# Performance work log

Measured on AMD Instinct MI355X. Metric: run time of the kernel, lower is better.

The kernel has to match this reference:

```python
import jax, jax.numpy as jnp
import numpy as np

B, C, H, W = 16, 512, 32, 32
KC = C // 8  # key_channels = 64


def setup_inputs() -> dict:
    key = jax.random.key(0)
    ks = jax.random.split(key, 6)
    s_in = 1.0 / np.sqrt(C)
    return {
        "x": jax.random.normal(ks[0], (B, C, H, W), dtype=jnp.float32),
        "Wq": jax.random.normal(ks[1], (KC, C), dtype=jnp.float32) * s_in,
        "bq": jnp.zeros((KC,), dtype=jnp.float32),
        "Wk": jax.random.normal(ks[2], (KC, C), dtype=jnp.float32) * s_in,
        "bk": jnp.zeros((KC,), dtype=jnp.float32),
        "Wv": jax.random.normal(ks[3], (C, C), dtype=jnp.float32) * s_in,
        "bv": jnp.zeros((C,), dtype=jnp.float32),
        "Wo": jax.random.normal(ks[4], (C, C), dtype=jnp.float32) * s_in,
        "bo": jnp.zeros((C,), dtype=jnp.float32),
        "gamma": jnp.zeros((1,), dtype=jnp.float32),
    }


def reference(x, Wq, bq, Wk, bk, Wv, bv, Wo, bo, gamma):
    b, c, h, w = x.shape
    n = h * w
    kc = Wq.shape[0]
    xf = x.reshape(b, c, n)  # [B, C, N]
    # 1x1 convs == channel matmuls
    q = jnp.einsum('kc,bcn->bnk', Wq, xf) + bq  # [B, N, KC]
    k = jnp.einsum('kc,bcn->bkn', Wk, xf) + bk[None, :, None]  # [B, KC, N]
    v = jnp.einsum('vc,bcn->bnv', Wv, xf) + bv  # [B, N, C]
    scale = jnp.asarray(kc, x.dtype) ** -0.5
    att = jax.nn.softmax(jnp.einsum('bnk,bkm->bnm', q, k) * scale, axis=-1)  # [B, N, N]
    out = jnp.einsum('bnm,bmv->bnv', att, v)  # [B, N, C]
    out = jnp.einsum('cv,bnv->bcn', Wo, out) + bo[None, :, None]  # [B, C, N]
    out = gamma[0] * out + xf
    return out.reshape(b, c, h, w)
```

## Files before the change

kernel.cpp:

```cpp
#include <hip/hip_runtime.h>
#include <cstddef>


typedef unsigned short ushort_t;
typedef __attribute__((ext_vector_type(8))) short bf16x8;
typedef __attribute__((ext_vector_type(4))) float f32x4;
typedef __attribute__((ext_vector_type(2))) float f32x2;
typedef __attribute__((ext_vector_type(2))) unsigned u32x2;

#define QSCALE 0.18033688011112042f

__device__ __forceinline__ ushort_t f2bf_t(float f) {
  return (ushort_t)(__float_as_uint(f) >> 16);
}
__device__ __forceinline__ unsigned pk2bf(float lo, float hi) {
  return __builtin_amdgcn_perm(__float_as_uint(hi), __float_as_uint(lo),
                               0x07060302u);
}

__device__ __forceinline__ void gload16(const ushort_t* g, ushort_t* l) {
  __builtin_amdgcn_global_load_lds(
      (const __attribute__((address_space(1))) void*)g,
      (__attribute__((address_space(3))) void*)l, 16, 0, 0);
}

__device__ __forceinline__ void gemm512(
    const ushort_t* __restrict__ A, int lda,
    const ushort_t* __restrict__ B, int ldb,
    int m0, int n0, ushort_t* As, ushort_t* Bs, f32x4 (*acc)[2])
{
  const int t = threadIdx.x;
  const int lane = t & 63, quad = lane >> 4, l15 = lane & 15;
  const int w = t >> 6, wm = w >> 2, wn4 = w & 3;
  const int rr = (lane >> 3) & 7;
  const int gg = (lane & 7) ^ rr;

  #pragma unroll
  for (int i = 0; i < 4; ++i)
    #pragma unroll
    for (int j = 0; j < 2; ++j) acc[i][j] = (f32x4){0.f, 0.f, 0.f, 0.f};

  for (int k0 = 0; k0 < 512; k0 += 64) {
    __syncthreads();
    #pragma unroll
    for (int i = 0; i < 2; ++i) {
      const int mrow = w * 16 + i * 8;
      gload16(A + (size_t)(m0 + mrow + rr) * lda + k0 + gg * 8, As + mrow * 64);
      gload16(B + (size_t)(n0 + mrow + rr) * ldb + k0 + gg * 8, Bs + mrow * 64);
    }
    __syncthreads();
    #pragma unroll
    for (int kk = 0; kk < 2; ++kk) {
      const int gq = kk * 4 + quad;
      const int sg = (gq ^ (l15 & 7)) * 8;
      bf16x8 af[4], bfr[2];
      #pragma unroll
      for (int i = 0; i < 4; ++i)
        af[i] = *(const bf16x8*)(As + (wm * 64 + i * 16 + l15) * 64 + sg);
      #pragma unroll
      for (int j = 0; j < 2; ++j)
        bfr[j] = *(const bf16x8*)(Bs + (wn4 * 32 + j * 16 + l15) * 64 + sg);
      #pragma unroll
      for (int i = 0; i < 4; ++i)
        #pragma unroll
        for (int j = 0; j < 2; ++j)
          acc[i][j] = __builtin_amdgcn_mfma_f32_16x16x32_bf16(
              af[i], bfr[j], acc[i][j], 0, 0, 0);
    }
  }
  __syncthreads();
}

template <class F>
__device__ __forceinline__ void store_bf16_512(
    ushort_t* lds, ushort_t* __restrict__ out, int ldo, int m0, int n0,
    f32x4 (*acc)[2], F f)
{
  const int t = threadIdx.x;
  const int lane = t & 63, quad = lane >> 4, l15 = lane & 15;
  const int w = t >> 6, wm = w >> 2, wn4 = w & 3;
  #pragma unroll
  for (int i = 0; i < 4; ++i)
    #pragma unroll
    for (int j = 0; j < 2; ++j)
      #pragma unroll
      for (int r = 0; r < 4; ++r) {
        const int rl = wm * 64 + i * 16 + quad * 4 + r;
        const int cl = wn4 * 32 + j * 16 + l15;
        lds[rl * 136 + cl] = f2bf_t(f(i, j, r, acc[i][j][r]));
      }
  __syncthreads();
  #pragma unroll
  for (int i = 0; i < 4; ++i) {
    const int s = i * 512 + t, m = s >> 4, g = s & 15;
    const uint4 v = *(const uint4*)(lds + m * 136 + g * 8);
    *(uint4*)(out + (size_t)(m0 + m) * ldo + n0 + g * 8) = v;
  }
}

__global__ __launch_bounds__(256) void prep_x(
    const float* __restrict__ x,
    const float* __restrict__ Wq, const float* __restrict__ Wk,
    const float* __restrict__ Wv, const float* __restrict__ Wo,
    ushort_t* __restrict__ xbfT, ushort_t* __restrict__ Wqk,
    ushort_t* __restrict__ Wvb, ushort_t* __restrict__ Wob)
{
  __shared__ float T[64 * 66];
  const int t = threadIdx.x;
  if (blockIdx.y == 8) {
    const int id = blockIdx.z * 16 + blockIdx.x;
    #pragma unroll
    for (int p = 0; p < 5; ++p) {
      const int s = p * 256 + t;
      if (s < 1152) {
        const int u = id * 1152 + s;
        const int e = u * 2;
        float f0, f1;
        if (e < 32768)       { f0 = Wq[e];         f1 = Wq[e + 1]; }
        else if (e < 65536)  { f0 = Wk[e - 32768]; f1 = Wk[e - 32767]; }
        else if (e < 327680) { f0 = Wv[e - 65536]; f1 = Wv[e - 65535]; }
        else                 { f0 = Wo[e - 327680]; f1 = Wo[e - 327679]; }
        const unsigned pk = pk2bf(f0, f1);
        if (e < 65536)       *((unsigned*)Wqk + u) = pk;
        else if (e < 327680) *((unsigned*)Wvb + (u - 32768)) = pk;
        else                 *((unsigned*)Wob + (u - 163840)) = pk;
      }
    }
    return;
  }
  const int b = blockIdx.z, c0 = blockIdx.y * 64, n0 = blockIdx.x * 64;
  const float* xb = x + ((size_t)b * 512 + c0) * 1024 + n0;
  const int njf = t & 15, ci0 = t >> 4;
  #pragma unroll
  for (int p = 0; p < 4; ++p) {
    const int ci = p * 16 + ci0;
    const f32x4 v = *(const f32x4*)(xb + (size_t)ci * 1024 + njf * 4);
    float* d = &T[ci * 66 + njf * 4];
    *(f32x2*)(d)     = (f32x2){v[0], v[1]};
    *(f32x2*)(d + 2) = (f32x2){v[2], v[3]};
  }
  __syncthreads();
  const int c4 = (t & 15) * 4, nr0 = t >> 4;
  #pragma unroll
  for (int p = 0; p < 4; ++p) {
    const int nr = p * 16 + nr0;
    const float a0 = T[(c4 + 0) * 66 + nr];
    const float a1 = T[(c4 + 1) * 66 + nr];
    const float a2 = T[(c4 + 2) * 66 + nr];
    const float a3 = T[(c4 + 3) * 66 + nr];
    const u32x2 pkv = {pk2bf(a0, a1), pk2bf(a2, a3)};
    *(u32x2*)&xbfT[((size_t)b * 1024 + n0 + nr) * 512 + c0 + c4] = pkv;
  }
}

__global__ __launch_bounds__(512) void k1_fused(
    const ushort_t* __restrict__ xbfT, const ushort_t* __restrict__ Wqk,
    const ushort_t* __restrict__ Wvb,
    const float* __restrict__ bq, const float* __restrict__ bk,
    const float* __restrict__ bv,
    ushort_t* __restrict__ qkt, ushort_t* __restrict__ vt2)
{
  __shared__ __align__(16) ushort_t lds[17408];
  const unsigned lin = blockIdx.x;
  const unsigned wid = (lin & 7) * 80 + (lin >> 3);
  const int b = wid / 40, r = wid % 40;
  const int t = threadIdx.x, lane = t & 63, quad = lane >> 4, l15 = lane & 15;
  const int w = t >> 6, wm = w >> 2, wn4 = w & 3;
  f32x4 acc[4][2];
  if (r < 32) {
    const int m0 = (r >> 3) * 128, n0 = (r & 7) * 128;
    gemm512(Wvb, 512, xbfT + (size_t)b * 524288, 512, m0, n0,
            lds, lds + 8192, acc);
    float br[4][4];
    #pragma unroll
    for (int i = 0; i < 4; ++i)
      #pragma unroll
      for (int r2 = 0; r2 < 4; ++r2)
        br[i][r2] = bv[m0 + wm * 64 + i * 16 + quad * 4 + r2];
    store_bf16_512(lds, vt2 + (size_t)b * 524288, 1024, m0, n0, acc,
        [&](int i, int, int r2, float v) { return v + br[i][r2]; });
  } else {
    const int m0 = (r - 32) * 128;
    gemm512(xbfT + (size_t)b * 524288, 512, Wqk, 512, m0, 0,
            lds, lds + 8192, acc);
    float bc[2], qs[2];
    #pragma unroll
    for (int j = 0; j < 2; ++j) {
      const int col = wn4 * 32 + j * 16 + l15;
      bc[j] = (col < 64) ? bq[col] : bk[col - 64];
      qs[j] = (col < 64) ? QSCALE : 1.0f;
    }
    store_bf16_512(lds, qkt + (size_t)b * 131072, 128, m0, 0, acc,
        [&](int, int j, int, float v) { return (v + bc[j]) * qs[j]; });
  }
}

__global__ __launch_bounds__(512) void flash_attn(
    const ushort_t* __restrict__ qkt, const ushort_t* __restrict__ vt2,
    ushort_t* __restrict__ o1)
{
  __shared__ __align__(16) ushort_t buf[25088];
  __shared__ float lsum[64][4];
  ushort_t* Ks = buf;
  ushort_t* Vs = buf + 4096;
  ushort_t* Ps = buf + 20480;

  const int t = threadIdx.x;
  const int lane = t & 63, quad = lane >> 4, l15 = lane & 15;
  const int w = t >> 6, wm = w >> 2, wn4 = w & 3;
  const int rr = (lane >> 3) & 7, gg = (lane & 7) ^ rr;

  const unsigned lin = blockIdx.x;
  const unsigned wid = (lin & 7) * 64 + (lin >> 3);
  const int b  = wid >> 5;
  const int m0 = ((wid >> 1) & 15) * 64;
  const int c0 = (wid & 1) * 256;

  const ushort_t* qb = qkt + (size_t)b * 131072;
  const ushort_t* vb = vt2 + (size_t)b * 524288;

  gload16(qb + (size_t)(m0 + w * 8 + rr) * 128 + gg * 8, Ps + (w * 8) * 64);
  __syncthreads();
  bf16x8 af_q[2][2];
  #pragma unroll
  for (int kk = 0; kk < 2; ++kk) {
    const int sg = ((kk * 4 + quad) ^ (l15 & 7)) * 8;
    #pragma unroll
    for (int i = 0; i < 2; ++i)
      af_q[i][kk] = *(const bf16x8*)(Ps + (wm * 32 + i * 16 + l15) * 64 + sg);
  }

  f32x4 accO[2][4];
  #pragma unroll
  for (int i = 0; i < 2; ++i)
    #pragma unroll
    for (int j = 0; j < 4; ++j) accO[i][j] = (f32x4){0.f, 0.f, 0.f, 0.f};
  float rsum[2][4] = {{0.f, 0.f, 0.f, 0.f}, {0.f, 0.f, 0.f, 0.f}};

  ushort_t* ps_w = Ps + (wm * 32 + quad * 4) * 72 + wn4 * 16 + l15;
  const int sg0 = (quad ^ (l15 & 7)) * 8;
  const int sg1 = ((4 + quad) ^ (l15 & 7)) * 8;

  #pragma unroll 1
  for (int mc = 0; mc < 1024; mc += 64) {
    __syncthreads();
    gload16(qb + (size_t)(mc + w * 8 + rr) * 128 + 64 + gg * 8,
            Ks + (w * 8) * 64);
    #pragma unroll
    for (int i = 0; i < 4; ++i)
      gload16(vb + (size_t)(c0 + w * 32 + i * 8 + rr) * 1024 + mc + gg * 8,
              Vs + (w * 32 + i * 8) * 64);
    __syncthreads();

    f32x4 accS[2];
    accS[0] = (f32x4){0.f, 0.f, 0.f, 0.f};
    accS[1] = (f32x4){0.f, 0.f, 0.f, 0.f};
    #pragma unroll
    for (int kk = 0; kk < 2; ++kk) {
      const int sg = kk ? sg1 : sg0;
      const bf16x8 bk_ = *(const bf16x8*)(Ks + (wn4 * 16 + l15) * 64 + sg);
      #pragma unroll
      for (int i = 0; i < 2; ++i)
        accS[i] = __builtin_amdgcn_mfma_f32_16x16x32_bf16(
            af_q[i][kk], bk_, accS[i], 0, 0, 0);
    }
    #pragma unroll
    for (int i = 0; i < 2; ++i)
      #pragma unroll
      for (int r2 = 0; r2 < 4; ++r2) {
        const float e = __builtin_amdgcn_exp2f(accS[i][r2]);
        rsum[i][r2] += e;
        ps_w[(i * 16 + r2) * 72] = f2bf_t(e);
      }
    __syncthreads();

    #pragma unroll
    for (int kk = 0; kk < 2; ++kk) {
      const int gq = kk * 4 + quad;
      const int sgv = kk ? sg1 : sg0;
      bf16x8 ap[2], bv_[4];
      #pragma unroll
      for (int i = 0; i < 2; ++i)
        ap[i] = *(const bf16x8*)(Ps + (wm * 32 + i * 16 + l15) * 72 + gq * 8);
      #pragma unroll
      for (int j = 0; j < 4; ++j)
        bv_[j] = *(const bf16x8*)(Vs + (wn4 * 64 + j * 16 + l15) * 64 + sgv);
      #pragma unroll
      for (int i = 0; i < 2; ++i)
        #pragma unroll
        for (int j = 0; j < 4; ++j)
          accO[i][j] = __builtin_amdgcn_mfma_f32_16x16x32_bf16(
              ap[i], bv_[j], accO[i][j], 0, 0, 0);
    }
  }

  #pragma unroll
  for (int i = 0; i < 2; ++i)
    #pragma unroll
    for (int r2 = 0; r2 < 4; ++r2) {
      float s = rsum[i][r2];
      #pragma unroll
      for (int d = 1; d < 16; d <<= 1) s += __shfl_xor(s, d, 16);
      if (l15 == 0) lsum[wm * 32 + i * 16 + quad * 4 + r2][wn4] = s;
    }
  __syncthreads();

  ushort_t* fl_b = buf;
  #pragma unroll
  for (int i = 0; i < 2; ++i)
    #pragma unroll
    for (int r2 = 0; r2 < 4; ++r2) {
      const int row = wm * 32 + i * 16 + quad * 4 + r2;
      const float inv = 1.0f / (lsum[row][0] + lsum[row][1] +
                                lsum[row][2] + lsum[row][3]);
      #pragma unroll
      for (int j = 0; j < 4; ++j)
        fl_b[row * 264 + wn4 * 64 + j * 16 + l15] = f2bf_t(accO[i][j][r2] * inv);
    }
  __syncthreads();
  #pragma unroll
  for (int pp = 0; pp < 2; ++pp) {
    const int s = pp * 512 + t, m = s >> 4, g = s & 15;
    const uint4 v = *(const uint4*)(fl_b + m * 264 + g * 8);
    *(uint4*)(o1 + ((size_t)b * 1024 + m0 + m) * 512 + c0 + g * 8) = v;
  }
}

__global__ __launch_bounds__(512) void k4_proj(
    const ushort_t* __restrict__ Wob, const ushort_t* __restrict__ o1,
    const float* __restrict__ bo, const float* __restrict__ gamma,
    const float* __restrict__ x, float* __restrict__ out)
{
  __shared__ __align__(16) ushort_t lds[17408];
  const unsigned lin = blockIdx.x;
  const unsigned wid = (lin & 7) * 64 + (lin >> 3);
  const int b = wid >> 5, rem = wid & 31;
  const int m0 = (rem >> 3) * 128, n0 = (rem & 7) * 128;
  f32x4 acc[4][2];
  gemm512(Wob, 512, o1 + (size_t)b * 524288, 512, m0, n0,
          lds, lds + 8192, acc);
  const int t = threadIdx.x, lane = t & 63, quad = lane >> 4, l15 = lane & 15;
  const int w = t >> 6, wm = w >> 2, wn4 = w & 3;
  const float g = gamma[0];
  float br[4][4];
  #pragma unroll
  for (int i = 0; i < 4; ++i)
    #pragma unroll
    for (int r2 = 0; r2 < 4; ++r2)
      br[i][r2] = bo[m0 + wm * 64 + i * 16 + quad * 4 + r2];
  float* fl = (float*)lds;
  #pragma unroll
  for (int h = 0; h < 2; ++h) {
    if (wm == h) {
      #pragma unroll
      for (int i = 0; i < 4; ++i)
        #pragma unroll
        for (int j = 0; j < 2; ++j)
          #pragma unroll
          for (int r2 = 0; r2 < 4; ++r2)
            fl[(i * 16 + quad * 4 + r2) * 132 + wn4 * 32 + j * 16 + l15] =
                g * (acc[i][j][r2] + br[i][r2]);
    }
    __syncthreads();
    #pragma unroll
    for (int i2 = 0; i2 < 4; ++i2) {
      const int s = i2 * 512 + t, m = s >> 5, c4 = s & 31;
      f32x4 v = *(const f32x4*)(fl + m * 132 + c4 * 4);
      const size_t gi = ((size_t)b * 512 + m0 + h * 64 + m) * 1024 + n0 + c4 * 4;
      const f32x4 xr = *(const f32x4*)(x + gi);
      v += xr;
      *(f32x4*)(out + gi) = v;
    }
    __syncthreads();
  }
}

extern "C" void kernel_launch(void* const* d_in, const int* in_sizes, int n_in,
                              void* d_out, int out_size, void* d_ws, size_t ws_size,
                              hipStream_t stream) {
  const float* x     = (const float*)d_in[0];
  const float* Wq    = (const float*)d_in[1];
  const float* bq    = (const float*)d_in[2];
  const float* Wk    = (const float*)d_in[3];
  const float* bk    = (const float*)d_in[4];
  const float* Wv    = (const float*)d_in[5];
  const float* bv    = (const float*)d_in[6];
  const float* Wo    = (const float*)d_in[7];
  const float* bo    = (const float*)d_in[8];
  const float* gamma = (const float*)d_in[9];
  float* out = (float*)d_out;

  char* wsp = (char*)d_ws;
  ushort_t* xbfT   = (ushort_t*)wsp;  wsp += (size_t)16 * 1024 * 512 * 2;
  ushort_t* Wqk_bf = (ushort_t*)wsp;  wsp += (size_t)128 * 512 * 2;
  ushort_t* Wv_bf  = (ushort_t*)wsp;  wsp += (size_t)512 * 512 * 2;
  ushort_t* Wo_bf  = (ushort_t*)wsp;  wsp += (size_t)512 * 512 * 2;
  ushort_t* qkt    = (ushort_t*)wsp;  wsp += (size_t)16 * 1024 * 128 * 2;
  ushort_t* vt2    = (ushort_t*)wsp;  wsp += (size_t)16 * 512 * 1024 * 2;
  ushort_t* o1     = xbfT;

  prep_x    <<<dim3(16, 9, 16), 256, 0, stream>>>(x, Wq, Wk, Wv, Wo,
                                                  xbfT, Wqk_bf, Wv_bf, Wo_bf);
  k1_fused  <<<640, 512, 0, stream>>>(xbfT, Wqk_bf, Wv_bf, bq, bk, bv, qkt, vt2);
  flash_attn<<<512, 512, 0, stream>>>(qkt, vt2, o1);
  k4_proj   <<<512, 512, 0, stream>>>(Wo_bf, o1, bo, gamma, x, out);
}
```

Measured before the change: 162.4 us.

## Double flash-attention query tile to 128 rows per block for K/V reuse

Each flash_attn block now handles 128 query rows instead of 64, and the grid shrinks from 512 to 256 blocks. The warps are rearranged as 4x2 so each warp computes a 32x32 score tile and a 32x128 output tile. Each K/V chunk loaded into LDS is therefore reused by twice as many query rows, halving global K/V traffic. The epilogue writes the output in two 64-row halves to fit LDS. In exchange, each wave holds more accumulator registers and there are fewer blocks to spread across CUs, so latency may be harder to hide.

```diff
diff --git a/kernel.cpp b/kernel.cpp
--- a/kernel.cpp
+++ b/kernel.cpp
@@ -199,27 +199,31 @@
     const ushort_t* __restrict__ qkt, const ushort_t* __restrict__ vt2,
     ushort_t* __restrict__ o1)
 {
-  __shared__ __align__(16) ushort_t buf[25088];
-  __shared__ float lsum[64][4];
+  __shared__ __align__(16) ushort_t buf[29696];
+  __shared__ float lsum[128][2];
   ushort_t* Ks = buf;
   ushort_t* Vs = buf + 4096;
   ushort_t* Ps = buf + 20480;
 
   const int t = threadIdx.x;
   const int lane = t & 63, quad = lane >> 4, l15 = lane & 15;
-  const int w = t >> 6, wm = w >> 2, wn4 = w & 3;
+  const int w = t >> 6, wm = w >> 1, wn2 = w & 1;
   const int rr = (lane >> 3) & 7, gg = (lane & 7) ^ rr;
 
   const unsigned lin = blockIdx.x;
-  const unsigned wid = (lin & 7) * 64 + (lin >> 3);
-  const int b  = wid >> 5;
-  const int m0 = ((wid >> 1) & 15) * 64;
+  const unsigned wid = (lin & 7) * 32 + (lin >> 3);
+  const int b  = wid >> 4;
+  const int m0 = ((wid >> 1) & 7) * 128;
   const int c0 = (wid & 1) * 256;
 
   const ushort_t* qb = qkt + (size_t)b * 131072;
   const ushort_t* vb = vt2 + (size_t)b * 524288;
 
-  gload16(qb + (size_t)(m0 + w * 8 + rr) * 128 + gg * 8, Ps + (w * 8) * 64);
+  #pragma unroll
+  for (int i = 0; i < 2; ++i) {
+    const int row = w * 16 + i * 8;
+    gload16(qb + (size_t)(m0 + row + rr) * 128 + gg * 8, Ps + row * 64);
+  }
   __syncthreads();
   bf16x8 af_q[2][2];
   #pragma unroll
@@ -230,14 +234,14 @@
       af_q[i][kk] = *(const bf16x8*)(Ps + (wm * 32 + i * 16 + l15) * 64 + sg);
   }
 
-  f32x4 accO[2][4];
+  f32x4 accO[2][8];
   #pragma unroll
   for (int i = 0; i < 2; ++i)
     #pragma unroll
-    for (int j = 0; j < 4; ++j) accO[i][j] = (f32x4){0.f, 0.f, 0.f, 0.f};
+    for (int j = 0; j < 8; ++j) accO[i][j] = (f32x4){0.f, 0.f, 0.f, 0.f};
   float rsum[2][4] = {{0.f, 0.f, 0.f, 0.f}, {0.f, 0.f, 0.f, 0.f}};
 
-  ushort_t* ps_w = Ps + (wm * 32 + quad * 4) * 72 + wn4 * 16 + l15;
+  ushort_t* ps_w = Ps + (wm * 32 + quad * 4) * 72 + wn2 * 32 + l15;
   const int sg0 = (quad ^ (l15 & 7)) * 8;
   const int sg1 = ((4 + quad) ^ (l15 & 7)) * 8;
 
@@ -252,43 +256,52 @@
               Vs + (w * 32 + i * 8) * 64);
     __syncthreads();
 
-    f32x4 accS[2];
-    accS[0] = (f32x4){0.f, 0.f, 0.f, 0.f};
-    accS[1] = (f32x4){0.f, 0.f, 0.f, 0.f};
+    f32x4 accS[2][2];
+    #pragma unroll
+    for (int i = 0; i < 2; ++i)
+      #pragma unroll
+      for (int j = 0; j < 2; ++j) accS[i][j] = (f32x4){0.f, 0.f, 0.f, 0.f};
     #pragma unroll
     for (int kk = 0; kk < 2; ++kk) {
       const int sg = kk ? sg1 : sg0;
-      const bf16x8 bk_ = *(const bf16x8*)(Ks + (wn4 * 16 + l15) * 64 + sg);
+      bf16x8 bk_[2];
+      #pragma unroll
+      for (int j = 0; j < 2; ++j)
+        bk_[j] = *(const bf16x8*)(Ks + (wn2 * 32 + j * 16 + l15) * 64 + sg);
       #pragma unroll
       for (int i = 0; i < 2; ++i)
-        accS[i] = __builtin_amdgcn_mfma_f32_16x16x32_bf16(
-            af_q[i][kk], bk_, accS[i], 0, 0, 0);
+        #pragma unroll
+        for (int j = 0; j < 2; ++j)
+          accS[i][j] = __builtin_amdgcn_mfma_f32_16x16x32_bf16(
+              af_q[i][kk], bk_[j], accS[i][j], 0, 0, 0);
     }
     #pragma unroll
     for (int i = 0; i < 2; ++i)
       #pragma unroll
-      for (int r2 = 0; r2 < 4; ++r2) {
-        const float e = __builtin_amdgcn_exp2f(accS[i][r2]);
-        rsum[i][r2] += e;
-        ps_w[(i * 16 + r2) * 72] = f2bf_t(e);
-      }
+      for (int j = 0; j < 2; ++j)
+        #pragma unroll
+        for (int r2 = 0; r2 < 4; ++r2) {
+          const float e = __builtin_amdgcn_exp2f(accS[i][j][r2]);
+          rsum[i][r2] += e;
+          ps_w[(i * 16 + r2) * 72 + j * 16] = f2bf_t(e);
+        }
     __syncthreads();
 
     #pragma unroll
     for (int kk = 0; kk < 2; ++kk) {
       const int gq = kk * 4 + quad;
       const int sgv = kk ? sg1 : sg0;
-      bf16x8 ap[2], bv_[4];
+      bf16x8 ap[2], bv_[8];
       #pragma unroll
       for (int i = 0; i < 2; ++i)
         ap[i] = *(const bf16x8*)(Ps + (wm * 32 + i * 16 + l15) * 72 + gq * 8);
       #pragma unroll
-      for (int j = 0; j < 4; ++j)
-        bv_[j] = *(const bf16x8*)(Vs + (wn4 * 64 + j * 16 + l15) * 64 + sgv);
+      for (int j = 0; j < 8; ++j)
+        bv_[j] = *(const bf16x8*)(Vs + (wn2 * 128 + j * 16 + l15) * 64 + sgv);
       #pragma unroll
       for (int i = 0; i < 2; ++i)
         #pragma unroll
-        for (int j = 0; j < 4; ++j)
+        for (int j = 0; j < 8; ++j)
           accO[i][j] = __builtin_amdgcn_mfma_f32_16x16x32_bf16(
               ap[i], bv_[j], accO[i][j], 0, 0, 0);
     }
@@ -301,28 +314,34 @@
       float s = rsum[i][r2];
       #pragma unroll
       for (int d = 1; d < 16; d <<= 1) s += __shfl_xor(s, d, 16);
-      if (l15 == 0) lsum[wm * 32 + i * 16 + quad * 4 + r2][wn4] = s;
+      if (l15 == 0) lsum[wm * 32 + i * 16 + quad * 4 + r2][wn2] = s;
     }
   __syncthreads();
 
   ushort_t* fl_b = buf;
   #pragma unroll
-  for (int i = 0; i < 2; ++i)
-    #pragma unroll
-    for (int r2 = 0; r2 < 4; ++r2) {
-      const int row = wm * 32 + i * 16 + quad * 4 + r2;
-      const float inv = 1.0f / (lsum[row][0] + lsum[row][1] +
-                                lsum[row][2] + lsum[row][3]);
-      #pragma unroll
-      for (int j = 0; j < 4; ++j)
-        fl_b[row * 264 + wn4 * 64 + j * 16 + l15] = f2bf_t(accO[i][j][r2] * inv);
-    }
-  __syncthreads();
-  #pragma unroll
-  for (int pp = 0; pp < 2; ++pp) {
-    const int s = pp * 512 + t, m = s >> 4, g = s & 15;
-    const uint4 v = *(const uint4*)(fl_b + m * 264 + g * 8);
-    *(uint4*)(o1 + ((size_t)b * 1024 + m0 + m) * 512 + c0 + g * 8) = v;
+  for (int h = 0; h < 2; ++h) {
+    if ((wm >> 1) == h) {
+      #pragma unroll
+      for (int i = 0; i < 2; ++i)
+        #pragma unroll
+        for (int r2 = 0; r2 < 4; ++r2) {
+          const int row = wm * 32 + i * 16 + quad * 4 + r2;
+          const float inv = 1.0f / (lsum[row][0] + lsum[row][1]);
+          #pragma unroll
+          for (int j = 0; j < 8; ++j)
+            fl_b[(row - h * 64) * 264 + wn2 * 128 + j * 16 + l15] =
+                f2bf_t(accO[i][j][r2] * inv);
+        }
+    }
+    __syncthreads();
+    #pragma unroll
+    for (int pp = 0; pp < 4; ++pp) {
+      const int s = pp * 512 + t, m = s >> 5, g = s & 31;
+      const uint4 v = *(const uint4*)(fl_b + m * 264 + g * 8);
+      *(uint4*)(o1 + ((size_t)b * 1024 + m0 + h * 64 + m) * 512 + c0 + g * 8) = v;
+    }
+    __syncthreads();
   }
 }
 
@@ -402,6 +421,6 @@
   prep_x    <<<dim3(16, 9, 16), 256, 0, stream>>>(x, Wq, Wk, Wv, Wo,
                                                   xbfT, Wqk_bf, Wv_bf, Wo_bf);
   k1_fused  <<<640, 512, 0, stream>>>(xbfT, Wqk_bf, Wv_bf, bq, bk, bv, qkt, vt2);
-  flash_attn<<<512, 512, 0, stream>>>(qkt, vt2, o1);
+  flash_attn<<<256, 512, 0, stream>>>(qkt, vt2, o1);
   k4_proj   <<<512, 512, 0, stream>>>(Wo_bf, o1, bo, gamma, x, out);
 }
```

Result: slower. 168.6 us (+3.8%).
